# Kernel tuning notes

Measured on AMD Instinct MI355X. Metric: run time of the kernel, lower is better.

Reference implementation:

```python
import jax, jax.numpy as jnp
import numpy as np

N_HEAD = 16

def setup_inputs() -> dict:
    key = jax.random.key(0)
    k1, k2, k3 = jax.random.split(key, 3)
    B, T, C = 4, 2048, 1024
    x = jax.random.normal(k1, (B, T, C), dtype=jnp.float32)
    w_attn = jax.random.normal(k2, (C, 3 * C), dtype=jnp.float32) * (1.0 / np.sqrt(C))
    w_proj = jax.random.normal(k3, (C, C), dtype=jnp.float32) * (1.0 / np.sqrt(C))
    return {"x": x, "w_attn": w_attn, "w_proj": w_proj}

def reference(x, w_attn, w_proj):
    B, T, C = x.shape
    H = N_HEAD
    D = C // H
    qkv = x @ w_attn  # [B, T, 3C]
    q, k, v = jnp.split(qkv, 3, axis=2)
    # [B, H, T, D]
    q = q.reshape(B, T, H, D).transpose(0, 2, 1, 3)
    k = k.reshape(B, T, H, D).transpose(0, 2, 1, 3)
    v = v.reshape(B, T, H, D).transpose(0, 2, 1, 3)
    att = jnp.einsum('bhqd,bhkd->bhqk', q, k) * (1.0 / np.sqrt(D))
    causal = jnp.tril(jnp.ones((T, T), dtype=bool))
    att = jnp.where(causal[None, None, :, :], att, -jnp.inf)
    att = jax.nn.softmax(att, axis=-1)
    y = jnp.einsum('bhqk,bhkd->bhqd', att, v)  # [B, H, T, D]
    y = y.transpose(0, 2, 1, 3).reshape(B, T, C)
    return y @ w_proj
```

## Files before the change

### kernel.cpp

```cpp
#include <hip/hip_runtime.h>
#include <hip/hip_bf16.h>
#include <math.h>

#define B_   4
#define T_   2048
#define C_   1024
#define H_   16
#define D_   64
#define M_   (B_*T_)
#define N3   (3*C_)
#define KDIM C_

typedef __attribute__((ext_vector_type(8)))  short bf16x8;
typedef __attribute__((ext_vector_type(4)))  float f32x4;
typedef __attribute__((ext_vector_type(16))) float f32x16;
typedef __attribute__((ext_vector_type(4)))  unsigned int u32x4;

#define MFMA16(a,b,c) __builtin_amdgcn_mfma_f32_16x16x32_bf16(a,b,c,0,0,0)
#define MFMA32(a,b,c) __builtin_amdgcn_mfma_f32_32x32x16_bf16(a,b,c,0,0,0)

#define QSCALE 0.18033688011112042f

__device__ __forceinline__ unsigned short f2bf(float f) {
  union { float f; unsigned u; } a; a.f = f;
  unsigned r = a.u + 0x7fffu + ((a.u >> 16) & 1u);
  return (unsigned short)(r >> 16);
}

__device__ __forceinline__ unsigned cvtpk(float lo, float hi) {
  unsigned r;
  asm("v_cvt_pk_bf16_f32 %0, %1, %2" : "=v"(r) : "v"(lo), "v"(hi));
  return r;
}

__device__ __forceinline__ void gload16(const void* g, void* l) {
  __builtin_amdgcn_global_load_lds(
      (const __attribute__((address_space(1))) void*)g,
      (__attribute__((address_space(3))) void*)l, 16, 0, 0);
}

__global__ void cast_f32_bf16(const float* __restrict__ in,
                              unsigned short* __restrict__ out, int n) {
  int i = (blockIdx.x * 256 + threadIdx.x) * 4;
  if (i >= n) return;
  float4 v = *(const float4*)(in + i);
  ushort4 o;
  o.x = f2bf(v.x); o.y = f2bf(v.y); o.z = f2bf(v.z); o.w = f2bf(v.w);
  *(ushort4*)(out + i) = o;
}

__global__ void transpose_cast(const float* __restrict__ in,
                               unsigned short* __restrict__ out,
                               int R, int Ncols) {
  __shared__ float tile[32][33];
  int bc = blockIdx.x * 32;
  int br = blockIdx.y * 32;
  int tx = threadIdx.x, ty = threadIdx.y;
  #pragma unroll
  for (int i = ty; i < 32; i += 8)
    tile[i][tx] = in[(size_t)(br + i) * Ncols + bc + tx];
  __syncthreads();
  #pragma unroll
  for (int i = ty; i < 32; i += 8)
    out[(size_t)(bc + i) * R + br + tx] = f2bf(tile[tx][i]);
}

template<int MODE>
__global__ __launch_bounds__(256)
void gemm128(const unsigned short* __restrict__ A,
             const unsigned short* __restrict__ Bt,
             unsigned short* __restrict__ qo,
             unsigned short* __restrict__ ko,
             unsigned short* __restrict__ vto,
             float* __restrict__ outf) {
  __shared__ short Asl[128 * 64];
  __shared__ short Bsl[128 * 64];
  const int tid  = threadIdx.x;
  const int wid  = tid >> 6, lane = tid & 63;
  const int l15  = lane & 15, l4 = lane >> 4;
  const int tm   = blockIdx.y * 128;
  const int tn   = blockIdx.x * 128;
  const int wm   = (wid >> 1) * 64, wn = (wid & 1) * 64;

  f32x4 acc[4][4] = {};
  const int stoff = wid * 1024 + lane * 16;

  for (int kt = 0; kt < KDIM; kt += 64) {
    __syncthreads();
    #pragma unroll
    for (int ro = 0; ro < 4; ++ro) {
      int off = ro * 4096 + stoff;
      int row = off >> 7;
      int ce  = (off & 127) >> 1;
      gload16(A  + (size_t)(tm + row) * KDIM + kt + ce,
              (char*)Asl + ro * 4096 + wid * 1024);
      gload16(Bt + (size_t)(tn + row) * KDIM + kt + ce,
              (char*)Bsl + ro * 4096 + wid * 1024);
    }
    __syncthreads();

    #pragma unroll
    for (int ks = 0; ks < 2; ++ks) {
      bf16x8 af[4], bfr[4];
      #pragma unroll
      for (int i = 0; i < 4; ++i) {
        af[i]  = *(const bf16x8*)&Asl[(wm + i*16 + l15) * 64 + ks*32 + l4*8];
        bfr[i] = *(const bf16x8*)&Bsl[(wn + i*16 + l15) * 64 + ks*32 + l4*8];
      }
      #pragma unroll
      for (int mi = 0; mi < 4; ++mi)
        #pragma unroll
        for (int ni = 0; ni < 4; ++ni)
          acc[mi][ni] = MFMA16(af[mi], bfr[ni], acc[mi][ni]);
    }
  }

  #pragma unroll
  for (int mi = 0; mi < 4; ++mi) {
    #pragma unroll
    for (int ni = 0; ni < 4; ++ni) {
      #pragma unroll
      for (int r = 0; r < 4; ++r) {
        int m = tm + wm + mi*16 + l4*4 + r;
        int n = tn + wn + ni*16 + l15;
        float val = acc[mi][ni][r];
        if (MODE == 0) {
          int b = m >> 11, t = m & (T_ - 1);
          int which = n >> 10, n1 = n & (C_ - 1);
          int h = n1 >> 6, d = n1 & 63;
          size_t bh = (size_t)(b * H_ + h);
          if (which == 0)      qo[(bh * T_ + t) * D_ + d] = f2bf(val * QSCALE);
          else if (which == 1) ko[(bh * T_ + t) * D_ + d] = f2bf(val);
          else                 vto[(bh * D_ + d) * T_ + t] = f2bf(val);
        } else {
          outf[(size_t)m * C_ + n] = val;
        }
      }
    }
  }
}

__global__ __launch_bounds__(256)
void attn32(const unsigned short* __restrict__ Q,
            const unsigned short* __restrict__ K,
            const unsigned short* __restrict__ Vt,
            unsigned short* __restrict__ Y) {
  const int bh   = blockIdx.x;
  const int qb   = (int)gridDim.y - 1 - (int)blockIdx.y;
  const int lane = threadIdx.x & 63, w = threadIdx.x >> 6;
  const int l31  = lane & 31, hi = lane >> 5;
  const int q0   = qb * 128 + w * 32;
  const int b    = bh >> 4, h = bh & 15;

  const unsigned short* Qp = Q  + (size_t)bh * T_ * D_;
  const unsigned short* Kp = K  + (size_t)bh * T_ * D_;
  const unsigned short* Vp = Vt + (size_t)bh * D_ * T_;

  bf16x8 qf[4];
  #pragma unroll
  for (int c = 0; c < 4; ++c)
    qf[c] = *(const bf16x8*)&Qp[(size_t)(q0 + l31) * D_ + c*16 + hi*8];

  f32x16 acc[2] = {};
  float m_q = -INFINITY, l_q = 0.f;

  const int nt = (q0 + 31) / 64 + 1;
  for (int kt = 0; kt < nt; ++kt) {
    const int k0 = kt * 64;

    bf16x8 kf[2][4];
    #pragma unroll
    for (int kb = 0; kb < 2; ++kb)
      #pragma unroll
      for (int c = 0; c < 4; ++c)
        kf[kb][c] = *(const bf16x8*)&Kp[(size_t)(k0 + kb*32 + l31) * D_ + c*16 + hi*8];

    f32x16 s2[2] = {};
    #pragma unroll
    for (int c = 0; c < 4; ++c) s2[0] = MFMA32(kf[0][c], qf[c], s2[0]);
    #pragma unroll
    for (int c = 0; c < 4; ++c) s2[1] = MFMA32(kf[1][c], qf[c], s2[1]);

    bf16x8 va[2][4];
    #pragma unroll
    for (int dt = 0; dt < 2; ++dt)
      #pragma unroll
      for (int s = 0; s < 4; ++s)
        va[dt][s] = *(const bf16x8*)&Vp[(size_t)(dt*32 + l31) * T_ + k0 + s*16 + hi*8];

    if (kt == nt - 1) {
      #pragma unroll
      for (int kb = 0; kb < 2; ++kb)
        #pragma unroll
        for (int r = 0; r < 16; ++r) {
          int krow = k0 + kb*32 + (r&3) + 8*(r>>2) + 4*hi;
          if (krow > q0 + l31) s2[kb][r] = -INFINITY;
        }
    }

    float tmax = s2[0][0];
    #pragma unroll
    for (int kb = 0; kb < 2; ++kb)
      #pragma unroll
      for (int r = 0; r < 16; ++r) tmax = fmaxf(tmax, s2[kb][r]);
    tmax = fmaxf(tmax, __shfl_xor(tmax, 32, 64));
    float mn = fmaxf(m_q, tmax);
    float scale = exp2f(m_q - mn);
    m_q = mn;

    float rsum = 0.f;
    #pragma unroll
    for (int kb = 0; kb < 2; ++kb)
      #pragma unroll
      for (int r = 0; r < 16; ++r) {
        float p = exp2f(s2[kb][r] - mn);
        s2[kb][r] = p;
        rsum += p;
      }
    rsum += __shfl_xor(rsum, 32, 64);
    l_q = l_q * scale + rsum;

    #pragma unroll
    for (int r = 0; r < 16; ++r) { acc[0][r] *= scale; acc[1][r] *= scale; }

    u32x4 pb[4];
    #pragma unroll
    for (int kb = 0; kb < 2; ++kb)
      #pragma unroll
      for (int ss = 0; ss < 2; ++ss)
        #pragma unroll
        for (int b2 = 0; b2 < 2; ++b2) {
          unsigned ce = cvtpk(s2[kb][8*ss     + 2*b2], s2[kb][8*ss     + 2*b2 + 1]);
          unsigned co = cvtpk(s2[kb][8*ss + 4 + 2*b2], s2[kb][8*ss + 4 + 2*b2 + 1]);
          auto rr = __builtin_amdgcn_permlane32_swap(ce, co, false, false);
          pb[kb*2 + ss][b2]     = rr[0];
          pb[kb*2 + ss][2 + b2] = rr[1];
        }

    #pragma unroll
    for (int dt = 0; dt < 2; ++dt)
      #pragma unroll
      for (int s = 0; s < 4; ++s)
        acc[dt] = MFMA32(va[dt][s], __builtin_bit_cast(bf16x8, pb[s]), acc[dt]);
  }

  float inv = 1.0f / l_q;
  const int t = q0 + l31;
  unsigned short* Yrow = Y + ((size_t)b * T_ + t) * C_ + h * D_;
  #pragma unroll
  for (int dt = 0; dt < 2; ++dt)
    #pragma unroll
    for (int rg = 0; rg < 4; ++rg) {
      uint2 wv;
      wv.x = cvtpk(acc[dt][rg*4 + 0] * inv, acc[dt][rg*4 + 1] * inv);
      wv.y = cvtpk(acc[dt][rg*4 + 2] * inv, acc[dt][rg*4 + 3] * inv);
      *(uint2*)(Yrow + dt*32 + rg*8 + hi*4) = wv;
    }
}

extern "C" void kernel_launch(void* const* d_in, const int* in_sizes, int n_in,
                              void* d_out, int out_size, void* d_ws, size_t ws_size,
                              hipStream_t stream) {
  const float* x      = (const float*)d_in[0];
  const float* w_attn = (const float*)d_in[1];
  const float* w_proj = (const float*)d_in[2];
  float* out = (float*)d_out;

  char* ws = (char*)d_ws;
  size_t off = 0;
  auto alloc = [&](size_t bytes) {
    char* p = ws + off; off += (bytes + 255) & ~(size_t)255; return p;
  };
  unsigned short* xb  = (unsigned short*)alloc((size_t)M_ * C_ * 2);
  unsigned short* wat = (unsigned short*)alloc((size_t)N3 * KDIM * 2);
  unsigned short* wpt = (unsigned short*)alloc((size_t)C_ * C_ * 2);
  unsigned short* qb  = (unsigned short*)alloc((size_t)M_ * C_ * 2);
  unsigned short* kb  = (unsigned short*)alloc((size_t)M_ * C_ * 2);
  unsigned short* vtb = (unsigned short*)alloc((size_t)M_ * C_ * 2);
  unsigned short* yb  = (unsigned short*)alloc((size_t)M_ * C_ * 2);

  cast_f32_bf16<<<dim3(M_ * C_ / 1024), dim3(256), 0, stream>>>(x, xb, M_ * C_);
  transpose_cast<<<dim3(N3 / 32, KDIM / 32), dim3(32, 8), 0, stream>>>(w_attn, wat, KDIM, N3);
  transpose_cast<<<dim3(C_ / 32, C_ / 32), dim3(32, 8), 0, stream>>>(w_proj, wpt, C_, C_);

  gemm128<0><<<dim3(N3 / 128, M_ / 128), dim3(256), 0, stream>>>(xb, wat, qb, kb, vtb, nullptr);
  attn32<<<dim3(B_ * H_, T_ / 128), dim3(256), 0, stream>>>(qb, kb, vtb, yb);
  gemm128<1><<<dim3(C_ / 128, M_ / 128), dim3(256), 0, stream>>>(yb, wpt, nullptr, nullptr, nullptr, out);
}
```

Baseline: 354.0 us.

## Pair causal query tiles per block, prefetch K, lazy rescale, MFMA priority

Each attention block now handles two query tiles, one short and one long (pair and NQT-1-pair), which balances causal work across blocks and halves the grid. The K fragments for the next key tile are loaded into registers during the current iteration, so global load latency overlaps with the softmax and the PV MFMAs. Rescaling of the online softmax is skipped unless the running max grows by more than 8 in the log2 domain, which saves the exp and the accumulator multiplies on most iterations. s_setprio is raised around the MFMA groups. The costs are higher register pressure from the double-buffered K fragments and fewer, longer-running blocks (512 instead of 1024).

```diff
diff --git a/kernel.cpp b/kernel.cpp
--- a/kernel.cpp
+++ b/kernel.cpp
@@ -146,116 +146,149 @@
             const unsigned short* __restrict__ Vt,
             unsigned short* __restrict__ Y) {
   const int bh   = blockIdx.x;
-  const int qb   = (int)gridDim.y - 1 - (int)blockIdx.y;
+  const int pair = blockIdx.y;
   const int lane = threadIdx.x & 63, w = threadIdx.x >> 6;
   const int l31  = lane & 31, hi = lane >> 5;
-  const int q0   = qb * 128 + w * 32;
   const int b    = bh >> 4, h = bh & 15;
 
   const unsigned short* Qp = Q  + (size_t)bh * T_ * D_;
   const unsigned short* Kp = K  + (size_t)bh * T_ * D_;
   const unsigned short* Vp = Vt + (size_t)bh * D_ * T_;
 
-  bf16x8 qf[4];
-  #pragma unroll
-  for (int c = 0; c < 4; ++c)
-    qf[c] = *(const bf16x8*)&Qp[(size_t)(q0 + l31) * D_ + c*16 + hi*8];
-
-  f32x16 acc[2] = {};
-  float m_q = -INFINITY, l_q = 0.f;
-
-  const int nt = (q0 + 31) / 64 + 1;
-  for (int kt = 0; kt < nt; ++kt) {
-    const int k0 = kt * 64;
-
-    bf16x8 kf[2][4];
+  const int NQT = T_ / 128;
+
+  for (int half = 0; half < 2; ++half) {
+    const int qtile = half ? (NQT - 1 - pair) : pair;
+    const int q0 = qtile * 128 + w * 32;
+
+    bf16x8 qf[4];
+    #pragma unroll
+    for (int c = 0; c < 4; ++c)
+      qf[c] = *(const bf16x8*)&Qp[(size_t)(q0 + l31) * D_ + c*16 + hi*8];
+
+    f32x16 acc[2] = {};
+    float m_q = -INFINITY, l_q = 0.f;
+
+    const int nt = (q0 + 31) / 64 + 1;
+
+    bf16x8 kfc[2][4];
     #pragma unroll
     for (int kb = 0; kb < 2; ++kb)
       #pragma unroll
       for (int c = 0; c < 4; ++c)
-        kf[kb][c] = *(const bf16x8*)&Kp[(size_t)(k0 + kb*32 + l31) * D_ + c*16 + hi*8];
-
-    f32x16 s2[2] = {};
-    #pragma unroll
-    for (int c = 0; c < 4; ++c) s2[0] = MFMA32(kf[0][c], qf[c], s2[0]);
-    #pragma unroll
-    for (int c = 0; c < 4; ++c) s2[1] = MFMA32(kf[1][c], qf[c], s2[1]);
-
-    bf16x8 va[2][4];
+        kfc[kb][c] = *(const bf16x8*)&Kp[(size_t)(kb*32 + l31) * D_ + c*16 + hi*8];
+
+    for (int kt = 0; kt < nt; ++kt) {
+      const int k0 = kt * 64;
+
+      f32x16 s2[2] = {};
+      __builtin_amdgcn_s_setprio(1);
+      #pragma unroll
+      for (int c = 0; c < 4; ++c) s2[0] = MFMA32(kfc[0][c], qf[c], s2[0]);
+      #pragma unroll
+      for (int c = 0; c < 4; ++c) s2[1] = MFMA32(kfc[1][c], qf[c], s2[1]);
+      __builtin_amdgcn_s_setprio(0);
+
+      bf16x8 va[2][4];
+      #pragma unroll
+      for (int dt = 0; dt < 2; ++dt)
+        #pragma unroll
+        for (int s = 0; s < 4; ++s)
+          va[dt][s] = *(const bf16x8*)&Vp[(size_t)(dt*32 + l31) * T_ + k0 + s*16 + hi*8];
+
+      bf16x8 kfn[2][4];
+      const bool havenext = (kt + 1 < nt);
+      if (havenext) {
+        const int k1 = k0 + 64;
+        #pragma unroll
+        for (int kb = 0; kb < 2; ++kb)
+          #pragma unroll
+          for (int c = 0; c < 4; ++c)
+            kfn[kb][c] = *(const bf16x8*)&Kp[(size_t)(k1 + kb*32 + l31) * D_ + c*16 + hi*8];
+      }
+
+      if (kt == nt - 1) {
+        #pragma unroll
+        for (int kb = 0; kb < 2; ++kb)
+          #pragma unroll
+          for (int r = 0; r < 16; ++r) {
+            int krow = k0 + kb*32 + (r&3) + 8*(r>>2) + 4*hi;
+            if (krow > q0 + l31) s2[kb][r] = -INFINITY;
+          }
+      }
+
+      float tmax = s2[0][0];
+      #pragma unroll
+      for (int kb = 0; kb < 2; ++kb)
+        #pragma unroll
+        for (int r = 0; r < 16; ++r) tmax = fmaxf(tmax, s2[kb][r]);
+
+      if (!__all(tmax <= m_q + 8.0f)) {
+        float tm2 = fmaxf(tmax, __shfl_xor(tmax, 32, 64));
+        float mn  = fmaxf(m_q, tm2);
+        float scale = exp2f(m_q - mn);
+        m_q = mn;
+        l_q *= scale;
+        #pragma unroll
+        for (int r = 0; r < 16; ++r) { acc[0][r] *= scale; acc[1][r] *= scale; }
+      }
+
+      float rsum = 0.f;
+      #pragma unroll
+      for (int kb = 0; kb < 2; ++kb)
+        #pragma unroll
+        for (int r = 0; r < 16; ++r) {
+          float p = exp2f(s2[kb][r] - m_q);
+          s2[kb][r] = p;
+          rsum += p;
+        }
+      rsum += __shfl_xor(rsum, 32, 64);
+      l_q += rsum;
+
+      u32x4 pb[4];
+      #pragma unroll
+      for (int kb = 0; kb < 2; ++kb)
+        #pragma unroll
+        for (int ss = 0; ss < 2; ++ss)
+          #pragma unroll
+          for (int b2 = 0; b2 < 2; ++b2) {
+            unsigned ce = cvtpk(s2[kb][8*ss     + 2*b2], s2[kb][8*ss     + 2*b2 + 1]);
+            unsigned co = cvtpk(s2[kb][8*ss + 4 + 2*b2], s2[kb][8*ss + 4 + 2*b2 + 1]);
+            auto rr = __builtin_amdgcn_permlane32_swap(ce, co, false, false);
+            pb[kb*2 + ss][b2]     = rr[0];
+            pb[kb*2 + ss][2 + b2] = rr[1];
+          }
+
+      __builtin_amdgcn_s_setprio(1);
+      #pragma unroll
+      for (int dt = 0; dt < 2; ++dt)
+        #pragma unroll
+        for (int s = 0; s < 4; ++s)
+          acc[dt] = MFMA32(va[dt][s], __builtin_bit_cast(bf16x8, pb[s]), acc[dt]);
+      __builtin_amdgcn_s_setprio(0);
+
+      if (havenext) {
+        #pragma unroll
+        for (int kb = 0; kb < 2; ++kb)
+          #pragma unroll
+          for (int c = 0; c < 4; ++c)
+            kfc[kb][c] = kfn[kb][c];
+      }
+    }
+
+    float inv = 1.0f / l_q;
+    const int t = q0 + l31;
+    unsigned short* Yrow = Y + ((size_t)b * T_ + t) * C_ + h * D_;
     #pragma unroll
     for (int dt = 0; dt < 2; ++dt)
       #pragma unroll
-      for (int s = 0; s < 4; ++s)
-        va[dt][s] = *(const bf16x8*)&Vp[(size_t)(dt*32 + l31) * T_ + k0 + s*16 + hi*8];
-
-    if (kt == nt - 1) {
-      #pragma unroll
-      for (int kb = 0; kb < 2; ++kb)
-        #pragma unroll
-        for (int r = 0; r < 16; ++r) {
-          int krow = k0 + kb*32 + (r&3) + 8*(r>>2) + 4*hi;
-          if (krow > q0 + l31) s2[kb][r] = -INFINITY;
-        }
-    }
-
-    float tmax = s2[0][0];
-    #pragma unroll
-    for (int kb = 0; kb < 2; ++kb)
-      #pragma unroll
-      for (int r = 0; r < 16; ++r) tmax = fmaxf(tmax, s2[kb][r]);
-    tmax = fmaxf(tmax, __shfl_xor(tmax, 32, 64));
-    float mn = fmaxf(m_q, tmax);
-    float scale = exp2f(m_q - mn);
-    m_q = mn;
-
-    float rsum = 0.f;
-    #pragma unroll
-    for (int kb = 0; kb < 2; ++kb)
-      #pragma unroll
-      for (int r = 0; r < 16; ++r) {
-        float p = exp2f(s2[kb][r] - mn);
-        s2[kb][r] = p;
-        rsum += p;
-      }
-    rsum += __shfl_xor(rsum, 32, 64);
-    l_q = l_q * scale + rsum;
-
-    #pragma unroll
-    for (int r = 0; r < 16; ++r) { acc[0][r] *= scale; acc[1][r] *= scale; }
-
-    u32x4 pb[4];
-    #pragma unroll
-    for (int kb = 0; kb < 2; ++kb)
-      #pragma unroll
-      for (int ss = 0; ss < 2; ++ss)
-        #pragma unroll
-        for (int b2 = 0; b2 < 2; ++b2) {
-          unsigned ce = cvtpk(s2[kb][8*ss     + 2*b2], s2[kb][8*ss     + 2*b2 + 1]);
-          unsigned co = cvtpk(s2[kb][8*ss + 4 + 2*b2], s2[kb][8*ss + 4 + 2*b2 + 1]);
-          auto rr = __builtin_amdgcn_permlane32_swap(ce, co, false, false);
-          pb[kb*2 + ss][b2]     = rr[0];
-          pb[kb*2 + ss][2 + b2] = rr[1];
-        }
-
-    #pragma unroll
-    for (int dt = 0; dt < 2; ++dt)
-      #pragma unroll
-      for (int s = 0; s < 4; ++s)
-        acc[dt] = MFMA32(va[dt][s], __builtin_bit_cast(bf16x8, pb[s]), acc[dt]);
+      for (int rg = 0; rg < 4; ++rg) {
+        uint2 wv;
+        wv.x = cvtpk(acc[dt][rg*4 + 0] * inv, acc[dt][rg*4 + 1] * inv);
+        wv.y = cvtpk(acc[dt][rg*4 + 2] * inv, acc[dt][rg*4 + 3] * inv);
+        *(uint2*)(Yrow + dt*32 + rg*8 + hi*4) = wv;
+      }
   }
-
-  float inv = 1.0f / l_q;
-  const int t = q0 + l31;
-  unsigned short* Yrow = Y + ((size_t)b * T_ + t) * C_ + h * D_;
-  #pragma unroll
-  for (int dt = 0; dt < 2; ++dt)
-    #pragma unroll
-    for (int rg = 0; rg < 4; ++rg) {
-      uint2 wv;
-      wv.x = cvtpk(acc[dt][rg*4 + 0] * inv, acc[dt][rg*4 + 1] * inv);
-      wv.y = cvtpk(acc[dt][rg*4 + 2] * inv, acc[dt][rg*4 + 3] * inv);
-      *(uint2*)(Yrow + dt*32 + rg*8 + hi*4) = wv;
-    }
 }
 
 extern "C" void kernel_launch(void* const* d_in, const int* in_sizes, int n_in,
@@ -284,6 +317,6 @@
   transpose_cast<<<dim3(C_ / 32, C_ / 32), dim3(32, 8), 0, stream>>>(w_proj, wpt, C_, C_);
 
   gemm128<0><<<dim3(N3 / 128, M_ / 128), dim3(256), 0, stream>>>(xb, wat, qb, kb, vtb, nullptr);
-  attn32<<<dim3(B_ * H_, T_ / 128), dim3(256), 0, stream>>>(qb, kb, vtb, yb);
+  attn32<<<dim3(B_ * H_, T_ / 256), dim3(256), 0, stream>>>(qb, kb, vtb, yb);
   gemm128<1><<<dim3(C_ / 128, M_ / 128), dim3(256), 0, stream>>>(yb, wpt, nullptr, nullptr, nullptr, out);
 }
```

New measurement: 351.6 us. No clear change (-0.7%).
